# Kernel tuning notes

Hardware: AMD Instinct MI355X
Metric: run time of the kernel (lower is better)

The kernel has to match this reference:

```python
import jax, jax.numpy as jnp
import numpy as np

BETA = 1.0 - 0.01      # 1 - voltage_decay
THRESH = 1.0           # threshold_voltage; theta state is never updated in the
                       # original forward (theta1/theta2 stay at init=0), so the
                       # effective adaptive threshold is THRESH + 0 every step.
ALPHA = 2.0            # snntorch default ATan surrogate alpha

@jax.custom_vjp
def spike_fn(x):
    # Heaviside forward, ATan surrogate backward (snntorch default spike_grad)
    return (x > 0).astype(x.dtype)

def _spike_fwd(x):
    return (x > 0).astype(x.dtype), x

def _spike_bwd(x, g):
    return (g * (ALPHA / 2.0) / (1.0 + (jnp.pi / 2.0 * ALPHA * x) ** 2),)

spike_fn.defvjp(_spike_fwd, _spike_bwd)

def setup_inputs() -> dict:
    key = jax.random.key(0)
    k0, k1, k2 = jax.random.split(key, 3)
    B, T, D, H, A = 128, 32, 6400, 1000, 4
    x = jax.random.normal(k0, (B, T, D), jnp.float32)
    W1 = jax.random.normal(k1, (H, D), jnp.float32) * (1.0 / np.sqrt(D))
    b1 = jnp.zeros((H,), jnp.float32)
    W2 = jax.random.normal(k2, (A, H), jnp.float32) * (1.0 / np.sqrt(H))
    b2 = jnp.zeros((A,), jnp.float32)
    return {"x": x, "W1": W1, "b1": b1, "W2": W2, "b2": b2}

def _lif_step(mem, cur, thr):
    # snntorch Leaky, reset_mechanism='zero':
    #   reset based on PREVIOUS mem crossing threshold (detached),
    #   zeroes the whole new state (leaked mem + input) on reset step.
    reset = jax.lax.stop_gradient((mem > thr).astype(mem.dtype))
    mem_new = (BETA * mem + cur) * (1.0 - reset)
    spk = spike_fn(mem_new - thr)
    return spk, mem_new

def _snn_forward(x, W1, b1, W2, b2):
    B, T, _ = x.shape
    H, A = W1.shape[0], W2.shape[0]

    def step(carry, cur):
        mem1, mem2 = carry
        h1 = cur @ W1.T + b1                 # [B,H]
        spk1, mem1 = _lif_step(mem1, h1, THRESH)
        h2 = spk1 @ W2.T + b2                # [B,A]
        spk2, mem2 = _lif_step(mem2, h2, THRESH)
        return (mem1, mem2), spk2

    init = (jnp.zeros((B, H), x.dtype), jnp.zeros((B, A), x.dtype))
    xt = jnp.swapaxes(x, 0, 1)               # [T,B,D]
    _, spk2_rec = jax.lax.scan(step, init, xt)
    return jnp.swapaxes(spk2_rec, 0, 1)      # [B,T,A]

def reference(x, W1, b1, W2, b2):
    return _snn_forward(x, W1, b1, W2, b2)
```

## Files before the change

kernel.cpp:

```cpp
#include <hip/hip_runtime.h>
#include <hip/hip_bf16.h>

constexpr int Bn = 128;
constexpr int Tn = 32;
constexpr int Dn = 6400;
constexpr int Hn = 1000;
constexpr int An = 4;
constexpr int Mn = Bn * Tn;
constexpr int Npad = 1024;

constexpr int KS = Dn / 32;
constexpr int MC = Mn / 16;
constexpr int NC = Npad / 16;

typedef _Float16 half8 __attribute__((ext_vector_type(8)));
typedef _Float16 half4 __attribute__((ext_vector_type(4)));
typedef float floatx4 __attribute__((ext_vector_type(4)));

constexpr size_t H1_BYTES  = (size_t)Mn * Hn * 4;
constexpr size_t XS_BYTES  = (size_t)Mn * Dn * 2;
constexpr size_t WSp_BYTES = (size_t)Npad * Dn * 2;
constexpr size_t WS_R7     = H1_BYTES + 2 * XS_BYTES + 2 * WSp_BYTES;
constexpr size_t WS_SPLITK = 2 * H1_BYTES + 2 * XS_BYTES + 2 * WSp_BYTES;

__device__ __forceinline__ void async16(const void* g, void* l) {
    __builtin_amdgcn_global_load_lds(
        (const __attribute__((address_space(1))) void*)g,
        (__attribute__((address_space(3))) void*)l, 16, 0, 0);
}

__global__ __launch_bounds__(256)
void cvt2(const float* __restrict__ X, const float* __restrict__ W1,
          _Float16* __restrict__ Xh, _Float16* __restrict__ Xl,
          _Float16* __restrict__ Wh, _Float16* __restrict__ Wl)
{
    constexpr int LD2 = 264;
    __shared__ __align__(16) _Float16 hiS[16][LD2];
    __shared__ __align__(16) _Float16 loS[16][LD2];

    const int tid = threadIdx.x;
    const int lane = tid & 63;
    const int w = tid >> 6;
    const int bx = blockIdx.x;

    const float* src;
    _Float16 *dh, *dl;
    int c4, ks0, crow, nrows;
    if (bx < 256 * 25) {
        c4 = bx & 255; ks0 = (bx >> 8) * 8;
        src = X; dh = Xh; dl = Xl; crow = MC; nrows = 16;
    } else {
        const int b2 = bx - 256 * 25;
        c4 = b2 & 63; ks0 = (b2 >> 6) * 8;
        src = W1; dh = Wh; dl = Wl; crow = NC; nrows = Hn - c4 * 16;
    }

#pragma unroll
    for (int j = 0; j < 4; ++j) {
        const int row = w * 4 + j;
        float4 v = make_float4(0.f, 0.f, 0.f, 0.f);
        if (row < nrows)
            v = *(const float4*)(src + (size_t)(c4 * 16 + row) * Dn + ks0 * 32 + lane * 4);
        half4 hi, lo;
        hi[0] = (_Float16)v.x; lo[0] = (_Float16)((v.x - (float)hi[0]) * 4096.0f);
        hi[1] = (_Float16)v.y; lo[1] = (_Float16)((v.y - (float)hi[1]) * 4096.0f);
        hi[2] = (_Float16)v.z; lo[2] = (_Float16)((v.z - (float)hi[2]) * 4096.0f);
        hi[3] = (_Float16)v.w; lo[3] = (_Float16)((v.w - (float)hi[3]) * 4096.0f);
        *(half4*)&hiS[row][lane * 4] = hi;
        *(half4*)&loS[row][lane * 4] = lo;
    }
    __syncthreads();

    const int lr = lane & 15, lg = lane >> 4;
#pragma unroll
    for (int q = 0; q < 2; ++q) {
        const int ks = w * 2 + q;
        const size_t cbase = ((size_t)(ks0 + ks) * crow + c4) * 512;
        const half8 h = *(const half8*)&hiS[lr][ks * 32 + lg * 8];
        const half8 l = *(const half8*)&loS[lr][ks * 32 + lg * 8];
        *(half8*)(dh + cbase + lane * 8) = h;
        *(half8*)(dl + cbase + lane * 8) = l;
    }
}

__global__ __launch_bounds__(256, 2)
void gemm_sk2(const _Float16* __restrict__ Xh, const _Float16* __restrict__ Xl,
              const _Float16* __restrict__ Wh, const _Float16* __restrict__ Wl,
              float* __restrict__ H1)
{
    __shared__ __align__(16) _Float16 S[2][16][512];

    const int tid = threadIdx.x;
    const int lane = tid & 63;
    const int w = tid >> 6;
    const int kh = blockIdx.x & 1;
    const int nb = (blockIdx.x >> 1) & 7;
    const int mb = blockIdx.x >> 4;
    const int bm8 = mb * 8;
    const int bn8 = nb * 8;
    const int wm = w & 1;
    const int wn = w >> 1;
    const int ks0 = kh * (KS / 2);

    auto issueA = [&](int ks, int buf) {
        _Float16* base = &S[buf][0][0];
#pragma unroll
        for (int r = 0; r < 2; ++r) {
            const int i = w * 2 + r;
            const size_t ga = ((size_t)(ks * MC + bm8 + i)) * 512 + lane * 8;
            async16(Xh + ga, base + (0 + i) * 512);
            async16(Xl + ga, base + (8 + i) * 512);
        }
    };

    const _Float16* bhp = Wh + ((size_t)(ks0 * NC + bn8 + wn * 4)) * 512 + lane * 8;
    const _Float16* blp = Wl + ((size_t)(ks0 * NC + bn8 + wn * 4)) * 512 + lane * 8;
    constexpr size_t BSTEP = (size_t)NC * 512;

    floatx4 acc0[4][4] = {};
    floatx4 acc1[4][4] = {};

    issueA(ks0, 0);
    for (int it = 0; it < KS / 2; ++it) {
        const int buf = it & 1;
        __syncthreads();
        if (it + 1 < KS / 2) issueA(ks0 + it + 1, buf ^ 1);

        half8 bh[4], bl[4];
        const size_t bo = (size_t)it * BSTEP;
#pragma unroll
        for (int nt = 0; nt < 4; ++nt) {
            bh[nt] = *(const half8*)(bhp + bo + nt * 512);
            bl[nt] = *(const half8*)(blp + bo + nt * 512);
        }

        half8 ah[4], al[4];
#pragma unroll
        for (int mt = 0; mt < 4; ++mt) {
            ah[mt] = *(const half8*)&S[buf][wm * 4 + mt][lane * 8];
            al[mt] = *(const half8*)&S[buf][8 + wm * 4 + mt][lane * 8];
        }

#pragma unroll
        for (int mt = 0; mt < 4; ++mt)
#pragma unroll
            for (int nt = 0; nt < 4; ++nt) {
                acc0[mt][nt] = __builtin_amdgcn_mfma_f32_16x16x32_f16(ah[mt], bh[nt], acc0[mt][nt], 0, 0, 0);
                acc1[mt][nt] = __builtin_amdgcn_mfma_f32_16x16x32_f16(ah[mt], bl[nt], acc1[mt][nt], 0, 0, 0);
                acc1[mt][nt] = __builtin_amdgcn_mfma_f32_16x16x32_f16(al[mt], bh[nt], acc1[mt][nt], 0, 0, 0);
            }
    }

    float* H1o = H1 + (size_t)kh * ((size_t)Mn * Hn);
    const int fr = lane & 15;
    const int fq = lane >> 4;
#pragma unroll
    for (int nt = 0; nt < 4; ++nt) {
        const int n = nb * 128 + wn * 64 + nt * 16 + fr;
        if (n >= Hn) continue;
#pragma unroll
        for (int mt = 0; mt < 4; ++mt) {
            const int m = mb * 128 + wm * 64 + mt * 16 + fq * 4;
#pragma unroll
            for (int r = 0; r < 4; ++r)
                H1o[(size_t)(m + r) * Hn + n] =
                    acc0[mt][nt][r] + acc1[mt][nt][r] * (1.0f / 4096.0f);
        }
    }
}

constexpr int AH = 0;
constexpr int AL = 8 * 512;
constexpr int BH = 16 * 512;
constexpr int BL = 20 * 512;
constexpr int BUFSZ = 24 * 512;

__global__ __launch_bounds__(256, 2)
void gemm_frag2(const _Float16* __restrict__ Xh, const _Float16* __restrict__ Xl,
                const _Float16* __restrict__ Wh, const _Float16* __restrict__ Wl,
                float* __restrict__ H1)
{
    __shared__ __align__(16) _Float16 S[2 * BUFSZ];

    const int tid = threadIdx.x;
    const int lane = tid & 63;
    const int w = tid >> 6;
    const int nb = blockIdx.x & 15;
    const int mb = blockIdx.x >> 4;
    const int bm4 = mb * 8;
    const int bn4 = nb * 4;
    const int wm = w & 1;
    const int wn = w >> 1;

    auto issue = [&](int ks, int buf) {
        _Float16* base = &S[buf * BUFSZ];
#pragma unroll
        for (int r = 0; r < 2; ++r) {
            const int i = w * 2 + r;
            const size_t ga = ((size_t)(ks * MC + bm4 + i)) * 512 + lane * 8;
            async16(Xh + ga, base + AH + i * 512);
            async16(Xl + ga, base + AL + i * 512);
        }
        const size_t gb = ((size_t)(ks * NC + bn4 + w)) * 512 + lane * 8;
        async16(Wh + gb, base + BH + w * 512);
        async16(Wl + gb, base + BL + w * 512);
    };

    floatx4 acc0[4][2] = {};
    floatx4 acc1[4][2] = {};

    issue(0, 0);
    for (int it = 0; it < KS; ++it) {
        const int buf = it & 1;
        __syncthreads();
        if (it + 1 < KS) issue(it + 1, buf ^ 1);

        const _Float16* base = &S[buf * BUFSZ];
        half8 ah[4], al[4], bh[2], bl[2];
#pragma unroll
        for (int mt = 0; mt < 4; ++mt) {
            ah[mt] = *(const half8*)(base + AH + (wm * 4 + mt) * 512 + lane * 8);
            al[mt] = *(const half8*)(base + AL + (wm * 4 + mt) * 512 + lane * 8);
        }
#pragma unroll
        for (int nt = 0; nt < 2; ++nt) {
            bh[nt] = *(const half8*)(base + BH + (wn * 2 + nt) * 512 + lane * 8);
            bl[nt] = *(const half8*)(base + BL + (wn * 2 + nt) * 512 + lane * 8);
        }
#pragma unroll
        for (int mt = 0; mt < 4; ++mt)
#pragma unroll
            for (int nt = 0; nt < 2; ++nt) {
                acc0[mt][nt] = __builtin_amdgcn_mfma_f32_16x16x32_f16(ah[mt], bh[nt], acc0[mt][nt], 0, 0, 0);
                acc1[mt][nt] = __builtin_amdgcn_mfma_f32_16x16x32_f16(ah[mt], bl[nt], acc1[mt][nt], 0, 0, 0);
                acc1[mt][nt] = __builtin_amdgcn_mfma_f32_16x16x32_f16(al[mt], bh[nt], acc1[mt][nt], 0, 0, 0);
            }
    }

    const int fr = lane & 15;
    const int fq = lane >> 4;
#pragma unroll
    for (int nt = 0; nt < 2; ++nt) {
        const int n = nb * 64 + wn * 32 + nt * 16 + fr;
        if (n >= Hn) continue;
#pragma unroll
        for (int mt = 0; mt < 4; ++mt) {
            const int m = mb * 128 + wm * 64 + mt * 16 + fq * 4;
#pragma unroll
            for (int r = 0; r < 4; ++r)
                H1[(size_t)(m + r) * Hn + n] =
                    acc0[mt][nt][r] + acc1[mt][nt][r] * (1.0f / 4096.0f);
        }
    }
}

__global__ __launch_bounds__(256, 4)
void gemm_fb(const float* __restrict__ X, const float* __restrict__ W1,
             float* __restrict__ H1)
{
    constexpr int K = Dn;
    constexpr int LD = 72;
    __shared__ __align__(16) _Float16 As[2][64][LD];
    __shared__ __align__(16) _Float16 Bs[2][64][LD];

    const int tid = threadIdx.x;
    const int bm = blockIdx.x * 64;
    const int bn = blockIdx.y * 64;
    const int lane = tid & 63;
    const int wid = tid >> 6;
    const int wm = (wid & 1) * 32;
    const int wn = (wid >> 1) * 32;
    const int fr = lane & 15;
    const int fq = lane >> 4;

    const int row0 = tid >> 3;
    const int row1 = (tid + 256) >> 3;
    const int k8_0 = (tid & 7) * 8;

    float4 rx[2][2], rw[2][2];
    const float zero4[4] = {0.f, 0.f, 0.f, 0.f};

    auto load_tiles = [&](int k0) {
        rx[0][0] = *(const float4*)(X + (size_t)(bm + row0) * K + k0 + k8_0);
        rx[0][1] = *(const float4*)(X + (size_t)(bm + row0) * K + k0 + k8_0 + 4);
        rx[1][0] = *(const float4*)(X + (size_t)(bm + row1) * K + k0 + k8_0);
        rx[1][1] = *(const float4*)(X + (size_t)(bm + row1) * K + k0 + k8_0 + 4);
        const int n0 = bn + row0, n1 = bn + row1;
        if (n0 < Hn) {
            rw[0][0] = *(const float4*)(W1 + (size_t)n0 * K + k0 + k8_0);
            rw[0][1] = *(const float4*)(W1 + (size_t)n0 * K + k0 + k8_0 + 4);
        } else { rw[0][0] = *(const float4*)zero4; rw[0][1] = *(const float4*)zero4; }
        if (n1 < Hn) {
            rw[1][0] = *(const float4*)(W1 + (size_t)n1 * K + k0 + k8_0);
            rw[1][1] = *(const float4*)(W1 + (size_t)n1 * K + k0 + k8_0 + 4);
        } else { rw[1][0] = *(const float4*)zero4; rw[1][1] = *(const float4*)zero4; }
    };

    load_tiles(0);
    floatx4 acc0[2][2] = {};
    floatx4 acc1[2][2] = {};

    for (int k0 = 0; k0 < K; k0 += 64) {
#pragma unroll
        for (int p = 0; p < 2; ++p) {
            const int row = p ? row1 : row0;
            float v[8];
            *(float4*)&v[0] = rx[p][0]; *(float4*)&v[4] = rx[p][1];
            half8 hi, lo;
#pragma unroll
            for (int j = 0; j < 8; ++j) {
                hi[j] = (_Float16)v[j];
                lo[j] = (_Float16)((v[j] - (float)hi[j]) * 4096.0f);
            }
            *(half8*)&As[0][row][k8_0] = hi;
            *(half8*)&As[1][row][k8_0] = lo;

            *(float4*)&v[0] = rw[p][0]; *(float4*)&v[4] = rw[p][1];
#pragma unroll
            for (int j = 0; j < 8; ++j) {
                hi[j] = (_Float16)v[j];
                lo[j] = (_Float16)((v[j] - (float)hi[j]) * 4096.0f);
            }
            *(half8*)&Bs[0][row][k8_0] = hi;
            *(half8*)&Bs[1][row][k8_0] = lo;
        }
        __syncthreads();
        if (k0 + 64 < K) load_tiles(k0 + 64);

#pragma unroll
        for (int c = 0; c < 2; ++c) {
            half8 ahi[2], alo[2], bhi[2], blo[2];
#pragma unroll
            for (int mt = 0; mt < 2; ++mt) {
                ahi[mt] = *(const half8*)&As[0][wm + mt * 16 + fr][c * 32 + fq * 8];
                alo[mt] = *(const half8*)&As[1][wm + mt * 16 + fr][c * 32 + fq * 8];
            }
#pragma unroll
            for (int nt = 0; nt < 2; ++nt) {
                bhi[nt] = *(const half8*)&Bs[0][wn + nt * 16 + fr][c * 32 + fq * 8];
                blo[nt] = *(const half8*)&Bs[1][wn + nt * 16 + fr][c * 32 + fq * 8];
            }
#pragma unroll
            for (int mt = 0; mt < 2; ++mt)
#pragma unroll
                for (int nt = 0; nt < 2; ++nt) {
                    acc0[mt][nt] = __builtin_amdgcn_mfma_f32_16x16x32_f16(ahi[mt], bhi[nt], acc0[mt][nt], 0, 0, 0);
                    acc1[mt][nt] = __builtin_amdgcn_mfma_f32_16x16x32_f16(ahi[mt], blo[nt], acc1[mt][nt], 0, 0, 0);
                    acc1[mt][nt] = __builtin_amdgcn_mfma_f32_16x16x32_f16(alo[mt], bhi[nt], acc1[mt][nt], 0, 0, 0);
                }
        }
        __syncthreads();
    }

#pragma unroll
    for (int nt = 0; nt < 2; ++nt) {
        const int n = bn + wn + nt * 16 + fr;
        if (n >= Hn) continue;
#pragma unroll
        for (int mt = 0; mt < 2; ++mt) {
            const int m = bm + wm + mt * 16 + fq * 4;
#pragma unroll
            for (int r = 0; r < 4; ++r)
                H1[(size_t)(m + r) * Hn + n] =
                    acc0[mt][nt][r] + acc1[mt][nt][r] * (1.0f / 4096.0f);
        }
    }
}

__global__ __launch_bounds__(1024)
void snn_scan(const float* __restrict__ H1, const float* __restrict__ b1,
              const float* __restrict__ W2, const float* __restrict__ b2,
              float* __restrict__ out, int split)
{
    const int b = blockIdx.x;
    const int tid = threadIdx.x;
    const int lane = tid & 63;
    const int wid = tid >> 6;
    const bool act = (tid < Hn);
    constexpr size_t MH = (size_t)Mn * Hn;

    __shared__ float w2s[1024][5];
    __shared__ unsigned smask[1024];
    __shared__ float h2s[Tn][An];

#pragma unroll
    for (int a = 0; a < An; ++a)
        w2s[tid][a] = act ? W2[a * Hn + tid] : 0.f;

    const float b1v = act ? b1[tid] : 0.f;

    float cur[Tn];
#pragma unroll
    for (int t = 0; t < Tn; ++t) {
        const size_t idx = ((size_t)b * Tn + t) * Hn + tid;
        float c = act ? H1[idx] : 0.f;
        if (split && act) c += H1[idx + MH];
        cur[t] = c + b1v;
    }

    unsigned mask = 0;
    float mem1 = 0.f;
#pragma unroll
    for (int t = 0; t < Tn; ++t) {
        const float reset = (mem1 > 1.0f) ? 1.0f : 0.0f;
        mem1 = (0.99f * mem1 + cur[t]) * (1.0f - reset);
        if (mem1 > 1.0f) mask |= (1u << t);
    }
    smask[tid] = act ? mask : 0u;
    __syncthreads();

#pragma unroll
    for (int tt = 0; tt < 2; ++tt) {
        const int t = wid * 2 + tt;
        float p[An] = {0.f, 0.f, 0.f, 0.f};
        for (int h = lane; h < 1024; h += 64) {
            const float g = (smask[h] >> t) & 1u ? 1.0f : 0.0f;
#pragma unroll
            for (int a = 0; a < An; ++a) p[a] += g * w2s[h][a];
        }
#pragma unroll
        for (int off = 32; off > 0; off >>= 1)
#pragma unroll
            for (int a = 0; a < An; ++a) p[a] += __shfl_down(p[a], off, 64);
        if (lane == 0) {
#pragma unroll
            for (int a = 0; a < An; ++a) h2s[t][a] = p[a];
        }
    }
    __syncthreads();

    if (tid < An) {
        const float bias = b2[tid];
        float mem2 = 0.f;
#pragma unroll
        for (int t = 0; t < Tn; ++t) {
            const float h2 = h2s[t][tid] + bias;
            const float reset = (mem2 > 1.0f) ? 1.0f : 0.0f;
            mem2 = (0.99f * mem2 + h2) * (1.0f - reset);
            out[((size_t)b * Tn + t) * An + tid] = (mem2 > 1.0f) ? 1.0f : 0.0f;
        }
    }
}

extern "C" void kernel_launch(void* const* d_in, const int* in_sizes, int n_in,
                              void* d_out, int out_size, void* d_ws, size_t ws_size,
                              hipStream_t stream) {
    const float* x  = (const float*)d_in[0];
    const float* W1 = (const float*)d_in[1];
    const float* b1 = (const float*)d_in[2];
    const float* W2 = (const float*)d_in[3];
    const float* b2 = (const float*)d_in[4];
    float* out = (float*)d_out;

    char* ws = (char*)d_ws;
    float* H1 = (float*)ws;

    if (ws_size >= WS_SPLITK) {
        _Float16* Xh = (_Float16*)(ws + 2 * H1_BYTES);
        _Float16* Xl = (_Float16*)(ws + 2 * H1_BYTES + XS_BYTES);
        _Float16* Wh = (_Float16*)(ws + 2 * H1_BYTES + 2 * XS_BYTES);
        _Float16* Wl = (_Float16*)(ws + 2 * H1_BYTES + 2 * XS_BYTES + WSp_BYTES);

        cvt2<<<256 * 25 + 64 * 25, 256, 0, stream>>>(x, W1, Xh, Xl, Wh, Wl);
        gemm_sk2<<<512, 256, 0, stream>>>(Xh, Xl, Wh, Wl, H1);
        snn_scan<<<Bn, 1024, 0, stream>>>(H1, b1, W2, b2, out, 1);
    } else if (ws_size >= WS_R7) {
        _Float16* Xh = (_Float16*)(ws + H1_BYTES);
        _Float16* Xl = (_Float16*)(ws + H1_BYTES + XS_BYTES);
        _Float16* Wh = (_Float16*)(ws + H1_BYTES + 2 * XS_BYTES);
        _Float16* Wl = (_Float16*)(ws + H1_BYTES + 2 * XS_BYTES + WSp_BYTES);

        cvt2<<<256 * 25 + 64 * 25, 256, 0, stream>>>(x, W1, Xh, Xl, Wh, Wl);
        gemm_frag2<<<512, 256, 0, stream>>>(Xh, Xl, Wh, Wl, H1);
        snn_scan<<<Bn, 1024, 0, stream>>>(H1, b1, W2, b2, out, 0);
    } else {
        dim3 grid(Mn / 64, (Hn + 63) / 64);
        gemm_fb<<<grid, 256, 0, stream>>>(x, W1, H1);
        snn_scan<<<Bn, 1024, 0, stream>>>(H1, b1, W2, b2, out, 0);
    }
}
```

Before: 344.0 us.

## Deepen split-K GEMM pipeline with 4-stage LDS ring and B register prefetch

Replaces the double-buffered A tile loop with a 4-slot LDS ring that prefetches two K-steps ahead. It also double-buffers the B fragments in registers, loading the next step's B while computing the current one. Explicit vmcnt waits and raw s_barrier calls replace __syncthreads so that loads can stay in flight across iterations. This doubles LDS use and raises register pressure, which may hurt occupancy at two blocks per CU. The hand-set vmcnt(12) count must match the number of outstanding loads exactly, or correctness is at risk.

Result: slower. 447.4 us (+30.0%).

```diff
diff --git a/kernel.cpp b/kernel.cpp
--- a/kernel.cpp
+++ b/kernel.cpp
@@ -88,7 +88,7 @@
               const _Float16* __restrict__ Wh, const _Float16* __restrict__ Wl,
               float* __restrict__ H1)
 {
-    __shared__ __align__(16) _Float16 S[2][16][512];
+    __shared__ __align__(16) _Float16 S[4][16][512];
 
     const int tid = threadIdx.x;
     const int lane = tid & 63;
@@ -101,6 +101,7 @@
     const int wm = w & 1;
     const int wn = w >> 1;
     const int ks0 = kh * (KS / 2);
+    constexpr int NIT = KS / 2;
 
     auto issueA = [&](int ks, int buf) {
         _Float16* base = &S[buf][0][0];
@@ -120,36 +121,51 @@
     floatx4 acc0[4][4] = {};
     floatx4 acc1[4][4] = {};
 
-    issueA(ks0, 0);
-    for (int it = 0; it < KS / 2; ++it) {
-        const int buf = it & 1;
-        __syncthreads();
-        if (it + 1 < KS / 2) issueA(ks0 + it + 1, buf ^ 1);
-
-        half8 bh[4], bl[4];
-        const size_t bo = (size_t)it * BSTEP;
-#pragma unroll
-        for (int nt = 0; nt < 4; ++nt) {
-            bh[nt] = *(const half8*)(bhp + bo + nt * 512);
-            bl[nt] = *(const half8*)(blp + bo + nt * 512);
-        }
-
-        half8 ah[4], al[4];
-#pragma unroll
-        for (int mt = 0; mt < 4; ++mt) {
-            ah[mt] = *(const half8*)&S[buf][wm * 4 + mt][lane * 8];
-            al[mt] = *(const half8*)&S[buf][8 + wm * 4 + mt][lane * 8];
-        }
-
-#pragma unroll
-        for (int mt = 0; mt < 4; ++mt)
-#pragma unroll
-            for (int nt = 0; nt < 4; ++nt) {
-                acc0[mt][nt] = __builtin_amdgcn_mfma_f32_16x16x32_f16(ah[mt], bh[nt], acc0[mt][nt], 0, 0, 0);
-                acc1[mt][nt] = __builtin_amdgcn_mfma_f32_16x16x32_f16(ah[mt], bl[nt], acc1[mt][nt], 0, 0, 0);
-                acc1[mt][nt] = __builtin_amdgcn_mfma_f32_16x16x32_f16(al[mt], bh[nt], acc1[mt][nt], 0, 0, 0);
-            }
-    }
+    half8 bh0[4], bl0[4], bh1[4], bl1[4];
+
+    issueA(ks0 + 0, 0);
+    issueA(ks0 + 1, 1);
+#pragma unroll
+    for (int nt = 0; nt < 4; ++nt) {
+        bh0[nt] = *(const half8*)(bhp + nt * 512);
+        bl0[nt] = *(const half8*)(blp + nt * 512);
+    }
+
+#define SK2_BODY(IT, BUF, BHC, BLC, BHN, BLN)                                   \
+    {                                                                           \
+        asm volatile("s_waitcnt vmcnt(12)" ::: "memory");                       \
+        __builtin_amdgcn_sched_barrier(0);                                      \
+        __builtin_amdgcn_s_barrier();                                           \
+        __builtin_amdgcn_sched_barrier(0);                                      \
+        if ((IT) + 2 < NIT) issueA(ks0 + (IT) + 2, ((IT) + 2) & 3);             \
+        if ((IT) + 1 < NIT) {                                                   \
+            const size_t bo = (size_t)((IT) + 1) * BSTEP;                       \
+            _Pragma("unroll")                                                   \
+            for (int nt = 0; nt < 4; ++nt) {                                    \
+                BHN[nt] = *(const half8*)(bhp + bo + nt * 512);                 \
+                BLN[nt] = *(const half8*)(blp + bo + nt * 512);                 \
+            }                                                                   \
+        }                                                                       \
+        _Pragma("unroll")                                                       \
+        for (int mt = 0; mt < 4; ++mt) {                                        \
+            const half8 ah = *(const half8*)&S[BUF][wm * 4 + mt][lane * 8];     \
+            const half8 al = *(const half8*)&S[BUF][8 + wm * 4 + mt][lane * 8]; \
+            _Pragma("unroll")                                                   \
+            for (int nt = 0; nt < 4; ++nt) {                                    \
+                acc0[mt][nt] = __builtin_amdgcn_mfma_f32_16x16x32_f16(ah, BHC[nt], acc0[mt][nt], 0, 0, 0); \
+                acc1[mt][nt] = __builtin_amdgcn_mfma_f32_16x16x32_f16(ah, BLC[nt], acc1[mt][nt], 0, 0, 0); \
+                acc1[mt][nt] = __builtin_amdgcn_mfma_f32_16x16x32_f16(al, BHC[nt], acc1[mt][nt], 0, 0, 0); \
+            }                                                                   \
+        }                                                                       \
+    }
+
+    for (int it = 0; it < NIT; it += 4) {
+        SK2_BODY(it + 0, 0, bh0, bl0, bh1, bl1);
+        SK2_BODY(it + 1, 1, bh1, bl1, bh0, bl0);
+        SK2_BODY(it + 2, 2, bh0, bl0, bh1, bl1);
+        SK2_BODY(it + 3, 3, bh1, bl1, bh0, bl0);
+    }
+#undef SK2_BODY
 
     float* H1o = H1 + (size_t)kh * ((size_t)Mn * Hn);
     const int fr = lane & 15;
```
